# Kernel optimization log

Hardware: AMD Instinct MI355X
Metric: run time of the kernel (lower is better)

Reference implementation:

```python
import jax, jax.numpy as jnp
import numpy as np

THETA = 10000.0
NUM_HEADS = 16


def apply_rope(x, pos, theta):
    # x: [..., s, d_k] with d_k even; pos: [s] (broadcasts over leading dims)
    d_k = x.shape[-1]
    inv_freq = 1.0 / (theta ** (jnp.arange(0, d_k, 2, dtype=x.dtype) / d_k))  # [d_k/2]
    ang = pos.astype(x.dtype)[..., None] * inv_freq  # [s, d_k/2]
    cos, sin = jnp.cos(ang), jnp.sin(ang)
    xr = x.reshape(x.shape[:-1] + (d_k // 2, 2))
    x0, x1 = xr[..., 0], xr[..., 1]
    out0 = x0 * cos - x1 * sin
    out1 = x0 * sin + x1 * cos
    return jnp.stack((out0, out1), axis=-1).reshape(x.shape)


def setup_inputs() -> dict:
    key = jax.random.key(0)
    ks = jax.random.split(key, 5)
    B, S, D = 4, 2048, 1024
    sigma = 2.0 / (D + D) ** 0.5
    return {
        "x": jax.random.normal(ks[0], (B, S, D), dtype=jnp.float32),
        "token_positions": jnp.arange(S, dtype=jnp.int64 if jax.config.jax_enable_x64 else jnp.int32),
        "wq": jax.random.normal(ks[1], (D, D), dtype=jnp.float32) * sigma,
        "wk": jax.random.normal(ks[2], (D, D), dtype=jnp.float32) * sigma,
        "wv": jax.random.normal(ks[3], (D, D), dtype=jnp.float32) * sigma,
        "wo": jax.random.normal(ks[4], (D, D), dtype=jnp.float32) * sigma,
    }


def reference(x, token_positions, wq, wk, wv, wo):
    B, S, D = x.shape
    H = NUM_HEADS
    d_k = D // H

    def proj(w, t):  # weight [out, in], t [..., in]
        return jnp.einsum('oi,bsi->bso', w, t)

    def heads(t):  # [b, s, (h d)] -> [b, h, s, d]
        return t.reshape(B, S, H, d_k).transpose(0, 2, 1, 3)

    Q = heads(proj(wq, x))
    K = heads(proj(wk, x))
    V = heads(proj(wv, x))
    Q = apply_rope(Q, token_positions, THETA)
    K = apply_rope(K, token_positions, THETA)

    scores = jnp.einsum('bhqd,bhkd->bhqk', Q, K) * (d_k ** -0.5)
    causal = jnp.tril(jnp.ones((S, S), dtype=bool))
    scores = jnp.where(causal, scores, -jnp.inf)
    attn = jax.nn.softmax(scores.astype(jnp.float32), axis=-1).astype(scores.dtype)
    out = jnp.einsum('bhqk,bhkd->bhqd', attn, V)
    out = out.transpose(0, 2, 1, 3).reshape(B, S, D)
    return jnp.einsum('oi,bsi->bso', wo, out)
```

## Files before the change

### kernel.cpp

```cpp
#include <hip/hip_runtime.h>
#include <cstdint>
#include <cstddef>

#define Bv 4
#define Sv 2048
#define Hv 16
#define Dv 1024
#define Mv (Bv*Sv)

typedef __attribute__((ext_vector_type(8))) short short8;
typedef __attribute__((ext_vector_type(8))) unsigned short ushort8v;
typedef __attribute__((ext_vector_type(4))) float f32x4;

__device__ inline float bf2f(unsigned short u) {
  union { unsigned int i; float f; } x; x.i = ((unsigned int)u) << 16; return x.f;
}
__device__ inline unsigned short f2bf(float f) {
  union { float f; unsigned int i; } x; x.f = f;
  unsigned int r = x.i + 0x7FFFu + ((x.i >> 16) & 1u);
  return (unsigned short)(r >> 16);
}

typedef __attribute__((address_space(1))) const unsigned short gu16;
typedef __attribute__((address_space(3))) unsigned short lu16;
__device__ inline void gld_lds16(const unsigned short* g, unsigned short* l) {
  __builtin_amdgcn_global_load_lds((gu16*)g, (lu16*)l, 16, 0, 0);
}

__global__ __launch_bounds__(256) void prep_all(
    const float* __restrict__ x, const float* __restrict__ wq,
    const float* __restrict__ wk, const float* __restrict__ wv,
    const float* __restrict__ wo, const int* __restrict__ pos,
    unsigned short* __restrict__ xb, unsigned short* __restrict__ wqkvb,
    unsigned short* __restrict__ wob, float* __restrict__ tab) {
  const int bb = blockIdx.x, tid = threadIdx.x;
  if (bb < 8192) {
    int i = bb * 256 + tid;
    float4 v = reinterpret_cast<const float4*>(x)[i];
    ushort4 o;
    o.x = f2bf(v.x); o.y = f2bf(v.y); o.z = f2bf(v.z); o.w = f2bf(v.w);
    reinterpret_cast<ushort4*>(xb)[i] = o;
  } else if (bb < 11264) {
    int i = (bb - 8192) * 256 + tid;
    int w = i >> 18, off = i & 262143;
    const float* src = (w == 0) ? wq : (w == 1) ? wk : wv;
    float4 v = reinterpret_cast<const float4*>(src)[off];
    ushort4 o;
    o.x = f2bf(v.x); o.y = f2bf(v.y); o.z = f2bf(v.z); o.w = f2bf(v.w);
    reinterpret_cast<ushort4*>(wqkvb)[i] = o;
  } else if (bb < 12288) {
    int i = (bb - 11264) * 256 + tid;
    float4 v = reinterpret_cast<const float4*>(wo)[i];
    ushort4 o;
    o.x = f2bf(v.x); o.y = f2bf(v.y); o.z = f2bf(v.z); o.w = f2bf(v.w);
    reinterpret_cast<ushort4*>(wob)[i] = o;
  } else {
    int idx = (bb - 12288) * 256 + tid;
    int s = idx >> 5, i = idx & 31;
    float p = (float)pos[s];
    float a = p * __builtin_exp2f(-0.41524101186092027f * (float)i);
    tab[(s << 6) + i]      = __builtin_cosf(a);
    tab[(s << 6) + 32 + i] = __builtin_sinf(a);
  }
}

__device__ __forceinline__ void xcd_swizzle(int& bm, int& bn) {
  const int nx = gridDim.x;
  const int nwg = nx * gridDim.y;
  int flat = blockIdx.y * nx + blockIdx.x;
  if ((nwg & 7) == 0) {
    int q = nwg >> 3;
    flat = (flat & 7) * q + (flat >> 3);
  }
  bm = (flat / nx) * 128;
  bn = (flat % nx) * 128;
}

__device__ inline void storeC(float* p, float v) { *p = v; }
__device__ inline void storeC(unsigned short* p, float v) { *p = f2bf(v); }

template <typename CT>
__global__ __launch_bounds__(256) void gemm_bt_128(
    const unsigned short* __restrict__ A,
    const unsigned short* __restrict__ B,
    CT* __restrict__ C,
    int M, int N, int K) {
  __shared__ unsigned short As[128 * 64];
  __shared__ unsigned short Bs[128 * 64];
  const int tid = threadIdx.x;
  const int wave = tid >> 6, lane = tid & 63;
  int bm, bn;
  xcd_swizzle(bm, bn);
  const int wr = (wave >> 1) * 64, wc = (wave & 1) * 64;

  f32x4 acc[4][4] = {};

  int srow[4], scol[4];
#pragma unroll
  for (int i = 0; i < 4; ++i) {
    int c = i * 4 + wave;
    srow[i] = c * 8 + (lane >> 3);
    scol[i] = ((lane & 7) ^ ((lane >> 3) & 7)) * 8;
  }

  const int fr = lane & 15;
  const int g_ = lane >> 4;
  int offA[2][4], offB[2][4];
#pragma unroll
  for (int kh = 0; kh < 2; ++kh)
#pragma unroll
    for (int m = 0; m < 4; ++m) {
      offA[kh][m] = (wr + m * 16 + fr) * 64 + ((((kh << 2) + g_) ^ (fr & 7)) * 8);
      offB[kh][m] = (wc + m * 16 + fr) * 64 + ((((kh << 2) + g_) ^ (fr & 7)) * 8);
    }

  for (int k0 = 0; k0 < K; k0 += 64) {
#pragma unroll
    for (int i = 0; i < 4; ++i) {
      gld_lds16(A + (size_t)(bm + srow[i]) * K + k0 + scol[i], &As[(i * 4 + wave) * 512]);
      gld_lds16(B + (size_t)(bn + srow[i]) * K + k0 + scol[i], &Bs[(i * 4 + wave) * 512]);
    }
    __syncthreads();
#pragma unroll
    for (int kh = 0; kh < 2; ++kh) {
      short8 af[4], bfr[4];
#pragma unroll
      for (int m = 0; m < 4; m++)
        af[m] = *reinterpret_cast<const short8*>(&As[offA[kh][m]]);
#pragma unroll
      for (int n = 0; n < 4; n++)
        bfr[n] = *reinterpret_cast<const short8*>(&Bs[offB[kh][n]]);
#pragma unroll
      for (int m = 0; m < 4; m++)
#pragma unroll
        for (int n = 0; n < 4; n++)
          acc[m][n] = __builtin_amdgcn_mfma_f32_16x16x32_bf16(af[m], bfr[n], acc[m][n], 0, 0, 0);
    }
    __syncthreads();
  }

  const int er = (lane >> 4) * 4, ec = lane & 15;
#pragma unroll
  for (int m = 0; m < 4; m++)
#pragma unroll
    for (int n = 0; n < 4; n++)
#pragma unroll
      for (int r = 0; r < 4; r++) {
        int row = bm + wr + m * 16 + er + r;
        int col = bn + wc + n * 16 + ec;
        storeC(&C[(size_t)row * N + col], acc[m][n][r]);
      }
}

__global__ __launch_bounds__(256) void gemm_qkv(
    const unsigned short* __restrict__ A,
    const unsigned short* __restrict__ B,
    unsigned short* __restrict__ Qp,
    unsigned short* __restrict__ Kp,
    unsigned short* __restrict__ Vt,
    const float* __restrict__ tab) {
  const int K = Dv;
  __shared__ unsigned short As[128 * 64];
  __shared__ unsigned short Bs[128 * 64];
  const int tid = threadIdx.x;
  const int wave = tid >> 6, lane = tid & 63;
  int bm, bn;
  xcd_swizzle(bm, bn);
  const int wr = (wave >> 1) * 64, wc = (wave & 1) * 64;

  f32x4 acc[4][4] = {};

  int srow[4], scol[4];
#pragma unroll
  for (int i = 0; i < 4; ++i) {
    int c = i * 4 + wave;
    srow[i] = c * 8 + (lane >> 3);
    scol[i] = ((lane & 7) ^ ((lane >> 3) & 7)) * 8;
  }

  const int fr = lane & 15;
  const int g_ = lane >> 4;
  int offA[2][4], offB[2][4];
#pragma unroll
  for (int kh = 0; kh < 2; ++kh)
#pragma unroll
    for (int m = 0; m < 4; ++m) {
      offA[kh][m] = (wr + m * 16 + fr) * 64 + ((((kh << 2) + g_) ^ (fr & 7)) * 8);
      offB[kh][m] = (wc + m * 16 + fr) * 64 + ((((kh << 2) + g_) ^ (fr & 7)) * 8);
    }

  for (int k0 = 0; k0 < K; k0 += 64) {
#pragma unroll
    for (int i = 0; i < 4; ++i) {
      gld_lds16(A + (size_t)(bm + srow[i]) * K + k0 + scol[i], &As[(i * 4 + wave) * 512]);
      gld_lds16(B + (size_t)(bn + srow[i]) * K + k0 + scol[i], &Bs[(i * 4 + wave) * 512]);
    }
    __syncthreads();
#pragma unroll
    for (int kh = 0; kh < 2; ++kh) {
      short8 af[4], bfr[4];
#pragma unroll
      for (int m = 0; m < 4; m++)
        af[m] = *reinterpret_cast<const short8*>(&As[offA[kh][m]]);
#pragma unroll
      for (int n = 0; n < 4; n++)
        bfr[n] = *reinterpret_cast<const short8*>(&Bs[offB[kh][n]]);
#pragma unroll
      for (int m = 0; m < 4; m++)
#pragma unroll
        for (int n = 0; n < 4; n++)
          acc[m][n] = __builtin_amdgcn_mfma_f32_16x16x32_bf16(af[m], bfr[n], acc[m][n], 0, 0, 0);
    }
    __syncthreads();
  }

  const int er = (lane >> 4) * 4, ec = lane & 15;
  const int region = bn >> 10;
  if (region < 2) {
    unsigned short* T = (region == 0) ? Qp : Kp;
#pragma unroll
    for (int m = 0; m < 4; m++)
#pragma unroll
      for (int n = 0; n < 4; n++) {
        const int col = bn + wc + n * 16 + ec;
        const int ccol = col & (Dv - 1);
        const int ii = (ccol & 63) >> 1;
        const bool odd = col & 1;
#pragma unroll
        for (int r = 0; r < 4; r++) {
          int row = bm + wr + m * 16 + er + r;
          int s = row & (Sv - 1);
          float v = acc[m][n][r];
          float pv = __shfl_xor(v, 1);
          float cc = tab[(s << 6) + ii];
          float sn = tab[(s << 6) + 32 + ii];
          float o = odd ? __builtin_fmaf(pv, sn, v * cc)
                        : __builtin_fmaf(v, cc, -(pv * sn));
          T[(size_t)row * Dv + ccol] = f2bf(o);
        }
      }
  } else {
#pragma unroll
    for (int m = 0; m < 4; m++)
#pragma unroll
      for (int n = 0; n < 4; n++) {
        const int dfull = (bn - 2048) + wc + n * 16 + ec;
        const int row0 = bm + wr + m * 16 + er;
        const int bb = row0 >> 11, s = row0 & (Sv - 1);
        const size_t vtrow = ((size_t)bb * 16 + (dfull >> 6)) * 64 + (dfull & 63);
        ushort4 ov;
        ov.x = f2bf(acc[m][n][0]);
        ov.y = f2bf(acc[m][n][1]);
        ov.z = f2bf(acc[m][n][2]);
        ov.w = f2bf(acc[m][n][3]);
        *reinterpret_cast<ushort4*>(Vt + vtrow * Sv + s) = ov;
      }
  }
}

template <bool MASKED>
__device__ __forceinline__ void softmax_strip(
    f32x4 (&sacc)[2][4], const int qrel0,
    float (&mrun2)[2], float (&lrun)[2], f32x4 (&oacc)[2][4],
    unsigned int (&pk)[2][4][2]) {
  const float c1 = 0.18033688011112042f;
#pragma unroll
  for (int qf = 0; qf < 2; ++qf) {
    const int qrel = qrel0 + qf * 16;
    float pv[4][4];
    float mx = -INFINITY;
#pragma unroll
    for (int kf = 0; kf < 4; ++kf)
#pragma unroll
      for (int r = 0; r < 4; ++r) {
        float s = sacc[qf][kf][r];
        if (MASKED) s = (kf * 16 + r > qrel) ? -INFINITY : s;
        pv[kf][r] = s;
        mx = fmaxf(mx, s);
      }
    mx = fmaxf(mx, __shfl_xor(mx, 16));
    mx = fmaxf(mx, __shfl_xor(mx, 32));
    float pm = mx * c1;
    if (__any(pm > mrun2[qf] + 8.0f)) {
      float m2 = fmaxf(mrun2[qf], pm);
      float sfq = __builtin_exp2f(mrun2[qf] - m2);
      lrun[qf] *= sfq;
#pragma unroll
      for (int dc = 0; dc < 4; ++dc)
#pragma unroll
        for (int r = 0; r < 4; ++r) oacc[qf][dc][r] *= sfq;
      mrun2[qf] = m2;
    }
    const float nm = -mrun2[qf];
    float ps = 0.f;
#pragma unroll
    for (int kf = 0; kf < 4; ++kf)
#pragma unroll
      for (int r = 0; r < 4; ++r) {
        float p = __builtin_exp2f(__builtin_fmaf(pv[kf][r], c1, nm));
        ps += p;
        pv[kf][r] = p;
      }
    ps += __shfl_xor(ps, 16);
    ps += __shfl_xor(ps, 32);
    lrun[qf] += ps;
#pragma unroll
    for (int kf = 0; kf < 4; ++kf)
#pragma unroll
      for (int hh = 0; hh < 2; ++hh) {
        unsigned int rr;
        asm("v_cvt_pk_bf16_f32 %0, %1, %2"
            : "=v"(rr) : "v"(pv[kf][2 * hh]), "v"(pv[kf][2 * hh + 1]));
        pk[qf][kf][hh] = rr;
      }
  }
}

__device__ __forceinline__ void pv_strip(
    const short8 (&vfr)[2][4], const unsigned int (&pk)[2][4][2],
    f32x4 (&oacc)[2][4], const int idx0, const int idx1, const bool hi) {
#pragma unroll
  for (int ks = 0; ks < 2; ++ks)
#pragma unroll
    for (int qf = 0; qf < 2; ++qf) {
      int ra = __builtin_amdgcn_ds_bpermute(idx0, (int)pk[qf][2 * ks][0]);
      int rb = __builtin_amdgcn_ds_bpermute(idx0, (int)pk[qf][2 * ks + 1][0]);
      int rc = __builtin_amdgcn_ds_bpermute(idx0, (int)pk[qf][2 * ks][1]);
      int rd = __builtin_amdgcn_ds_bpermute(idx0, (int)pk[qf][2 * ks + 1][1]);
      int re = __builtin_amdgcn_ds_bpermute(idx1, (int)pk[qf][2 * ks][0]);
      int rf = __builtin_amdgcn_ds_bpermute(idx1, (int)pk[qf][2 * ks + 1][0]);
      int rg = __builtin_amdgcn_ds_bpermute(idx1, (int)pk[qf][2 * ks][1]);
      int rh = __builtin_amdgcn_ds_bpermute(idx1, (int)pk[qf][2 * ks + 1][1]);
      union { unsigned int u[4]; short8 v; } pw;
      pw.u[0] = hi ? (unsigned)rb : (unsigned)ra;
      pw.u[1] = hi ? (unsigned)rd : (unsigned)rc;
      pw.u[2] = hi ? (unsigned)rf : (unsigned)re;
      pw.u[3] = hi ? (unsigned)rh : (unsigned)rg;
      __builtin_amdgcn_s_setprio(1);
#pragma unroll
      for (int dc = 0; dc < 4; ++dc)
        oacc[qf][dc] = __builtin_amdgcn_mfma_f32_16x16x32_bf16(vfr[ks][dc], pw.v, oacc[qf][dc], 0, 0, 0);
      __builtin_amdgcn_s_setprio(0);
    }
}

__global__ __launch_bounds__(256, 2) void attn_mfma(
    const unsigned short* __restrict__ Q,
    const unsigned short* __restrict__ K,
    const unsigned short* __restrict__ Vt,
    unsigned short* __restrict__ O) {
  __shared__ __align__(16) unsigned short ldsK[3][4096];
  __shared__ __align__(16) unsigned short ldsV[3][4096];
  const int tid = threadIdx.x;
  const int wave = tid >> 6, lane = tid & 63;
  const int g = lane >> 4, m = lane & 15;
  const int F = blockIdx.x;
  const int q7 = F >> 3;
  const int bh = ((F & 7) << 3) | (q7 & 7);
  const int bi = q7 >> 3;
  const int b = bh >> 4, h = bh & 15;
  const int j = bi * 4 + wave;
  const int sA = j, sB = 63 - j;
  const int qA0 = sA * 32, qB0 = sB * 32;
  const int ntA = (sA >> 1) + 1, ntB = (sB >> 1) + 1;
  const int ntBmax = ((63 - bi * 4) >> 1) + 1;
  const size_t qkbase = ((size_t)b * Sv) * Dv + (size_t)h * 64;
  const size_t vtbase = (size_t)bh * 64 * Sv;
  const f32x4 zf = {0.f, 0.f, 0.f, 0.f};

  int srowS[2], scolS[2];
#pragma unroll
  for (int i = 0; i < 2; ++i) {
    int s = ((i * 4 + wave) << 6) + lane;
    int s2 = s ^ ((s >> 3) & 7);
    srowS[i] = s2 >> 3;
    scolS[i] = (s2 & 7) * 8;
  }

  short8 qA[2][2], qB[2][2];
#pragma unroll
  for (int qf = 0; qf < 2; ++qf)
#pragma unroll
    for (int ks = 0; ks < 2; ++ks) {
      qA[qf][ks] = *reinterpret_cast<const short8*>(
          Q + qkbase + (size_t)(qA0 + qf * 16 + m) * Dv + ks * 32 + g * 8);
      qB[qf][ks] = *reinterpret_cast<const short8*>(
          Q + qkbase + (size_t)(qB0 + qf * 16 + m) * Dv + ks * 32 + g * 8);
    }

  int offL[2][4];
#pragma unroll
  for (int ks = 0; ks < 2; ++ks)
#pragma unroll
    for (int f = 0; f < 4; ++f)
      offL[ks][f] = (f * 16 + m) * 64 + ((((ks << 2) + g) ^ (m & 7)) * 8);

  f32x4 oA[2][4] = {}, oB[2][4] = {};
  float mA[2] = {-INFINITY, -INFINITY}, mB[2] = {-INFINITY, -INFINITY};
  float lA[2] = {0.f, 0.f}, lB[2] = {0.f, 0.f};

  const int idx0 = (((g & 1) << 5) + m) << 2;
  const int idx1 = idx0 + 64;
  const bool hi = (g >= 2);
  int qrelA = qA0 + m - 4 * g;
  int qrelB = qB0 + m - 4 * g;

  auto STAGE = [&](int c, int t) {
    const int kb = t << 6;
#pragma unroll
    for (int i = 0; i < 2; ++i) {
      gld_lds16(K + qkbase + (size_t)(kb + srowS[i]) * Dv + scolS[i],
                &ldsK[c][(i * 4 + wave) * 512]);
      gld_lds16(Vt + vtbase + (size_t)srowS[i] * Sv + kb + scolS[i],
                &ldsV[c][(i * 4 + wave) * 512]);
    }
  };

  STAGE(0, 0);
  STAGE(1, 1);
  int cur = 0, bs = 2;

  for (int t = 0; t < ntBmax; ++t) {
    if (t + 1 < ntBmax) {
      asm volatile("s_waitcnt vmcnt(4)" ::: "memory");
    } else {
      asm volatile("s_waitcnt vmcnt(0)" ::: "memory");
    }
    __builtin_amdgcn_sched_barrier(0);
    __builtin_amdgcn_s_barrier();
    if (t + 2 < ntBmax) STAGE(bs, t + 2);

    if (t < ntB) {
      const bool actA = (t < ntA);
      f32x4 sAacc[2][4], sBacc[2][4];
      short8 kfr[4];
#pragma unroll
      for (int kf = 0; kf < 4; ++kf)
        kfr[kf] = *reinterpret_cast<const short8*>(&ldsK[cur][offL[0][kf]]);
      __builtin_amdgcn_s_setprio(1);
#pragma unroll
      for (int qf = 0; qf < 2; ++qf)
#pragma unroll
        for (int kf = 0; kf < 4; ++kf)
          sBacc[qf][kf] = __builtin_amdgcn_mfma_f32_16x16x32_bf16(kfr[kf], qB[qf][0], zf, 0, 0, 0);
      if (actA)
#pragma unroll
        for (int qf = 0; qf < 2; ++qf)
#pragma unroll
          for (int kf = 0; kf < 4; ++kf)
            sAacc[qf][kf] = __builtin_amdgcn_mfma_f32_16x16x32_bf16(kfr[kf], qA[qf][0], zf, 0, 0, 0);
      __builtin_amdgcn_s_setprio(0);
#pragma unroll
      for (int kf = 0; kf < 4; ++kf)
        kfr[kf] = *reinterpret_cast<const short8*>(&ldsK[cur][offL[1][kf]]);
      __builtin_amdgcn_s_setprio(1);
#pragma unroll
      for (int qf = 0; qf < 2; ++qf)
#pragma unroll
        for (int kf = 0; kf < 4; ++kf)
          sBacc[qf][kf] = __builtin_amdgcn_mfma_f32_16x16x32_bf16(kfr[kf], qB[qf][1], sBacc[qf][kf], 0, 0, 0);
      if (actA)
#pragma unroll
        for (int qf = 0; qf < 2; ++qf)
#pragma unroll
          for (int kf = 0; kf < 4; ++kf)
            sAacc[qf][kf] = __builtin_amdgcn_mfma_f32_16x16x32_bf16(kfr[kf], qA[qf][1], sAacc[qf][kf], 0, 0, 0);
      __builtin_amdgcn_s_setprio(0);

      short8 vfr[2][4];
#pragma unroll
      for (int ks = 0; ks < 2; ++ks)
#pragma unroll
        for (int dc = 0; dc < 4; ++dc)
          vfr[ks][dc] = *reinterpret_cast<const short8*>(&ldsV[cur][offL[ks][dc]]);

      unsigned int pkB[2][4][2], pkA[2][4][2];
      if (t == ntB - 1) softmax_strip<true >(sBacc, qrelB, mB, lB, oB, pkB);
      else              softmax_strip<false>(sBacc, qrelB, mB, lB, oB, pkB);
      if (actA) {
        if (t == ntA - 1) softmax_strip<true >(sAacc, qrelA, mA, lA, oA, pkA);
        else              softmax_strip<false>(sAacc, qrelA, mA, lA, oA, pkA);
      }
      pv_strip(vfr, pkB, oB, idx0, idx1, hi);
      if (actA) pv_strip(vfr, pkA, oA, idx0, idx1, hi);

      qrelA -= 64; qrelB -= 64;
    }

    cur = (cur == 2) ? 0 : cur + 1;
    bs = (bs == 2) ? 0 : bs + 1;
  }

#pragma unroll
  for (int qf = 0; qf < 2; ++qf) {
    float rnA = 1.0f / lA[qf];
    float rnB = 1.0f / lB[qf];
    size_t rowA = (size_t)(qA0 + qf * 16 + m);
    size_t rowB = (size_t)(qB0 + qf * 16 + m);
#pragma unroll
    for (int dc = 0; dc < 4; ++dc) {
      ushort4 ov;
      ov.x = f2bf(oA[qf][dc][0] * rnA);
      ov.y = f2bf(oA[qf][dc][1] * rnA);
      ov.z = f2bf(oA[qf][dc][2] * rnA);
      ov.w = f2bf(oA[qf][dc][3] * rnA);
      *reinterpret_cast<ushort4*>(O + qkbase + rowA * Dv + dc * 16 + 4 * g) = ov;
      ov.x = f2bf(oB[qf][dc][0] * rnB);
      ov.y = f2bf(oB[qf][dc][1] * rnB);
      ov.z = f2bf(oB[qf][dc][2] * rnB);
      ov.w = f2bf(oB[qf][dc][3] * rnB);
      *reinterpret_cast<ushort4*>(O + qkbase + rowB * Dv + dc * 16 + 4 * g) = ov;
    }
  }
}

extern "C" void kernel_launch(void* const* d_in, const int* in_sizes, int n_in,
                              void* d_out, int out_size, void* d_ws, size_t ws_size,
                              hipStream_t stream) {
  const float* x   = (const float*)d_in[0];
  const int*   pos = (const int*)d_in[1];
  const float* wq  = (const float*)d_in[2];
  const float* wk  = (const float*)d_in[3];
  const float* wv  = (const float*)d_in[4];
  const float* wo  = (const float*)d_in[5];
  float* out = (float*)d_out;

  char* w = (char*)d_ws;
  unsigned short* xb    = (unsigned short*)(w);
  unsigned short* wqkvb = (unsigned short*)(w + (16u << 20));
  unsigned short* wob   = (unsigned short*)(w + (22u << 20));
  unsigned short* Qp    = (unsigned short*)(w + (24u << 20));
  unsigned short* Kp    = (unsigned short*)(w + (40u << 20));
  unsigned short* Vt    = (unsigned short*)(w + (56u << 20));
  float*          tab   = (float*)(w + (72u << 20));

  prep_all<<<12544, 256, 0, stream>>>(x, wq, wk, wv, wo, pos, xb, wqkvb, wob, tab);

  gemm_qkv<<<dim3(3 * Dv / 128, Mv / 128), 256, 0, stream>>>(xb, wqkvb, Qp, Kp, Vt, tab);

  attn_mfma<<<512, 256, 0, stream>>>(Qp, Kp, Vt, xb);

  gemm_bt_128<float><<<dim3(Dv / 128, Mv / 128), 256, 0, stream>>>(xb, wob, out, Mv, Dv, Dv);
}
```

Before: 201.7 us.

## Split paired causal strips across separate waves with 512-thread attention blocks

The attention block grows from 4 to 8 waves. Each wave now handles a single 32-row query strip, where before one wave handled both a short and a long strip. Waves 0-3 take the front strips and waves 4-7 take the mirrored back strips, and each wave stages one K/V chunk per tile, so the vmcnt wait is adjusted to match. The goal is to halve per-wave register pressure and raise the number of resident waves, giving more latency hiding. The cost is that the short-strip waves sit idle at the barriers while the long-strip waves finish, which makes load imbalance inside a block worse.

```diff
diff --git a/kernel.cpp b/kernel.cpp
--- a/kernel.cpp
+++ b/kernel.cpp
@@ -344,7 +344,7 @@
     }
 }
 
-__global__ __launch_bounds__(256, 2) void attn_mfma(
+__global__ __launch_bounds__(512, 4) void attn_mfma(
     const unsigned short* __restrict__ Q,
     const unsigned short* __restrict__ K,
     const unsigned short* __restrict__ Vt,
@@ -359,34 +359,31 @@
   const int bh = ((F & 7) << 3) | (q7 & 7);
   const int bi = q7 >> 3;
   const int b = bh >> 4, h = bh & 15;
-  const int j = bi * 4 + wave;
-  const int sA = j, sB = 63 - j;
-  const int qA0 = sA * 32, qB0 = sB * 32;
-  const int ntA = (sA >> 1) + 1, ntB = (sB >> 1) + 1;
+  const int w4 = wave & 3;
+  const bool isB = wave >= 4;
+  const int strip = isB ? (63 - (bi * 4 + w4)) : (bi * 4 + w4);
+  const int q0 = strip * 32;
+  const int nt = (strip >> 1) + 1;
   const int ntBmax = ((63 - bi * 4) >> 1) + 1;
   const size_t qkbase = ((size_t)b * Sv) * Dv + (size_t)h * 64;
   const size_t vtbase = (size_t)bh * 64 * Sv;
   const f32x4 zf = {0.f, 0.f, 0.f, 0.f};
 
-  int srowS[2], scolS[2];
-#pragma unroll
-  for (int i = 0; i < 2; ++i) {
-    int s = ((i * 4 + wave) << 6) + lane;
+  int srowS, scolS;
+  {
+    int s = (wave << 6) + lane;
     int s2 = s ^ ((s >> 3) & 7);
-    srowS[i] = s2 >> 3;
-    scolS[i] = (s2 & 7) * 8;
-  }
-
-  short8 qA[2][2], qB[2][2];
+    srowS = s2 >> 3;
+    scolS = (s2 & 7) * 8;
+  }
+
+  short8 q[2][2];
 #pragma unroll
   for (int qf = 0; qf < 2; ++qf)
 #pragma unroll
-    for (int ks = 0; ks < 2; ++ks) {
-      qA[qf][ks] = *reinterpret_cast<const short8*>(
-          Q + qkbase + (size_t)(qA0 + qf * 16 + m) * Dv + ks * 32 + g * 8);
-      qB[qf][ks] = *reinterpret_cast<const short8*>(
-          Q + qkbase + (size_t)(qB0 + qf * 16 + m) * Dv + ks * 32 + g * 8);
-    }
+    for (int ks = 0; ks < 2; ++ks)
+      q[qf][ks] = *reinterpret_cast<const short8*>(
+          Q + qkbase + (size_t)(q0 + qf * 16 + m) * Dv + ks * 32 + g * 8);
 
   int offL[2][4];
 #pragma unroll
@@ -395,25 +392,21 @@
     for (int f = 0; f < 4; ++f)
       offL[ks][f] = (f * 16 + m) * 64 + ((((ks << 2) + g) ^ (m & 7)) * 8);
 
-  f32x4 oA[2][4] = {}, oB[2][4] = {};
-  float mA[2] = {-INFINITY, -INFINITY}, mB[2] = {-INFINITY, -INFINITY};
-  float lA[2] = {0.f, 0.f}, lB[2] = {0.f, 0.f};
+  f32x4 oacc[2][4] = {};
+  float mrun[2] = {-INFINITY, -INFINITY};
+  float lrun[2] = {0.f, 0.f};
 
   const int idx0 = (((g & 1) << 5) + m) << 2;
   const int idx1 = idx0 + 64;
   const bool hi = (g >= 2);
-  int qrelA = qA0 + m - 4 * g;
-  int qrelB = qB0 + m - 4 * g;
+  int qrel = q0 + m - 4 * g;
 
   auto STAGE = [&](int c, int t) {
     const int kb = t << 6;
-#pragma unroll
-    for (int i = 0; i < 2; ++i) {
-      gld_lds16(K + qkbase + (size_t)(kb + srowS[i]) * Dv + scolS[i],
-                &ldsK[c][(i * 4 + wave) * 512]);
-      gld_lds16(Vt + vtbase + (size_t)srowS[i] * Sv + kb + scolS[i],
-                &ldsV[c][(i * 4 + wave) * 512]);
-    }
+    gld_lds16(K + qkbase + (size_t)(kb + srowS) * Dv + scolS,
+              &ldsK[c][wave * 512]);
+    gld_lds16(Vt + vtbase + (size_t)srowS * Sv + kb + scolS,
+              &ldsV[c][wave * 512]);
   };
 
   STAGE(0, 0);
@@ -422,7 +415,7 @@
 
   for (int t = 0; t < ntBmax; ++t) {
     if (t + 1 < ntBmax) {
-      asm volatile("s_waitcnt vmcnt(4)" ::: "memory");
+      asm volatile("s_waitcnt vmcnt(2)" ::: "memory");
     } else {
       asm volatile("s_waitcnt vmcnt(0)" ::: "memory");
     }
@@ -430,9 +423,8 @@
     __builtin_amdgcn_s_barrier();
     if (t + 2 < ntBmax) STAGE(bs, t + 2);
 
-    if (t < ntB) {
-      const bool actA = (t < ntA);
-      f32x4 sAacc[2][4], sBacc[2][4];
+    if (t < nt) {
+      f32x4 sacc[2][4];
       short8 kfr[4];
 #pragma unroll
       for (int kf = 0; kf < 4; ++kf)
@@ -442,13 +434,7 @@
       for (int qf = 0; qf < 2; ++qf)
 #pragma unroll
         for (int kf = 0; kf < 4; ++kf)
-          sBacc[qf][kf] = __builtin_amdgcn_mfma_f32_16x16x32_bf16(kfr[kf], qB[qf][0], zf, 0, 0, 0);
-      if (actA)
-#pragma unroll
-        for (int qf = 0; qf < 2; ++qf)
-#pragma unroll
-          for (int kf = 0; kf < 4; ++kf)
-            sAacc[qf][kf] = __builtin_amdgcn_mfma_f32_16x16x32_bf16(kfr[kf], qA[qf][0], zf, 0, 0, 0);
+          sacc[qf][kf] = __builtin_amdgcn_mfma_f32_16x16x32_bf16(kfr[kf], q[qf][0], zf, 0, 0, 0);
       __builtin_amdgcn_s_setprio(0);
 #pragma unroll
       for (int kf = 0; kf < 4; ++kf)
@@ -458,13 +444,7 @@
       for (int qf = 0; qf < 2; ++qf)
 #pragma unroll
         for (int kf = 0; kf < 4; ++kf)
-          sBacc[qf][kf] = __builtin_amdgcn_mfma_f32_16x16x32_bf16(kfr[kf], qB[qf][1], sBacc[qf][kf], 0, 0, 0);
-      if (actA)
-#pragma unroll
-        for (int qf = 0; qf < 2; ++qf)
-#pragma unroll
-          for (int kf = 0; kf < 4; ++kf)
-            sAacc[qf][kf] = __builtin_amdgcn_mfma_f32_16x16x32_bf16(kfr[kf], qA[qf][1], sAacc[qf][kf], 0, 0, 0);
+          sacc[qf][kf] = __builtin_amdgcn_mfma_f32_16x16x32_bf16(kfr[kf], q[qf][1], sacc[qf][kf], 0, 0, 0);
       __builtin_amdgcn_s_setprio(0);
 
       short8 vfr[2][4];
@@ -474,17 +454,12 @@
         for (int dc = 0; dc < 4; ++dc)
           vfr[ks][dc] = *reinterpret_cast<const short8*>(&ldsV[cur][offL[ks][dc]]);
 
-      unsigned int pkB[2][4][2], pkA[2][4][2];
-      if (t == ntB - 1) softmax_strip<true >(sBacc, qrelB, mB, lB, oB, pkB);
-      else              softmax_strip<false>(sBacc, qrelB, mB, lB, oB, pkB);
-      if (actA) {
-        if (t == ntA - 1) softmax_strip<true >(sAacc, qrelA, mA, lA, oA, pkA);
-        else              softmax_strip<false>(sAacc, qrelA, mA, lA, oA, pkA);
-      }
-      pv_strip(vfr, pkB, oB, idx0, idx1, hi);
-      if (actA) pv_strip(vfr, pkA, oA, idx0, idx1, hi);
-
-      qrelA -= 64; qrelB -= 64;
+      unsigned int pk[2][4][2];
+      if (t == nt - 1) softmax_strip<true >(sacc, qrel, mrun, lrun, oacc, pk);
+      else             softmax_strip<false>(sacc, qrel, mrun, lrun, oacc, pk);
+      pv_strip(vfr, pk, oacc, idx0, idx1, hi);
+
+      qrel -= 64;
     }
 
     cur = (cur == 2) ? 0 : cur + 1;
@@ -493,23 +468,16 @@
 
 #pragma unroll
   for (int qf = 0; qf < 2; ++qf) {
-    float rnA = 1.0f / lA[qf];
-    float rnB = 1.0f / lB[qf];
-    size_t rowA = (size_t)(qA0 + qf * 16 + m);
-    size_t rowB = (size_t)(qB0 + qf * 16 + m);
+    float rn = 1.0f / lrun[qf];
+    size_t row = (size_t)(q0 + qf * 16 + m);
 #pragma unroll
     for (int dc = 0; dc < 4; ++dc) {
       ushort4 ov;
-      ov.x = f2bf(oA[qf][dc][0] * rnA);
-      ov.y = f2bf(oA[qf][dc][1] * rnA);
-      ov.z = f2bf(oA[qf][dc][2] * rnA);
-      ov.w = f2bf(oA[qf][dc][3] * rnA);
-      *reinterpret_cast<ushort4*>(O + qkbase + rowA * Dv + dc * 16 + 4 * g) = ov;
-      ov.x = f2bf(oB[qf][dc][0] * rnB);
-      ov.y = f2bf(oB[qf][dc][1] * rnB);
-      ov.z = f2bf(oB[qf][dc][2] * rnB);
-      ov.w = f2bf(oB[qf][dc][3] * rnB);
-      *reinterpret_cast<ushort4*>(O + qkbase + rowB * Dv + dc * 16 + 4 * g) = ov;
+      ov.x = f2bf(oacc[qf][dc][0] * rn);
+      ov.y = f2bf(oacc[qf][dc][1] * rn);
+      ov.z = f2bf(oacc[qf][dc][2] * rn);
+      ov.w = f2bf(oacc[qf][dc][3] * rn);
+      *reinterpret_cast<ushort4*>(O + qkbase + row * Dv + dc * 16 + 4 * g) = ov;
     }
   }
 }
@@ -538,7 +506,7 @@
 
   gemm_qkv<<<dim3(3 * Dv / 128, Mv / 128), 256, 0, stream>>>(xb, wqkvb, Qp, Kp, Vt, tab);
 
-  attn_mfma<<<512, 256, 0, stream>>>(Qp, Kp, Vt, xb);
+  attn_mfma<<<512, 512, 0, stream>>>(Qp, Kp, Vt, xb);
 
   gemm_bt_128<float><<<dim3(Dv / 128, Mv / 128), 256, 0, stream>>>(xb, wob, out, Mv, Dv, Dv);
 }
```

After: 276.2 us. +36.9%, slower.

## Overlap next K-tile global-to-LDS load with second-half MFMAs in GEMMs

Applied to the files above, without the earlier changes.

Restructures the K loop of the projection GEMMs so the second half-tile fragments are read into registers before a barrier. The next tile's direct global-to-LDS load is then issued while the last 16 MFMAs run on those registers, instead of loading only after all compute finishes. This hides part of the global load latency behind compute while keeping a single LDS buffer. It costs extra registers for the second fragment set, and the loop still has two barriers per tile.

```diff
diff --git a/kernel.cpp b/kernel.cpp
--- a/kernel.cpp
+++ b/kernel.cpp
@@ -114,28 +114,46 @@
       offB[kh][m] = (wc + m * 16 + fr) * 64 + ((((kh << 2) + g_) ^ (fr & 7)) * 8);
     }
 
-  for (int k0 = 0; k0 < K; k0 += 64) {
+  const int nt = K >> 6;
+  auto STAGE = [&](int t) {
+    const int k0 = t << 6;
 #pragma unroll
     for (int i = 0; i < 4; ++i) {
       gld_lds16(A + (size_t)(bm + srow[i]) * K + k0 + scol[i], &As[(i * 4 + wave) * 512]);
       gld_lds16(B + (size_t)(bn + srow[i]) * K + k0 + scol[i], &Bs[(i * 4 + wave) * 512]);
     }
+  };
+
+  STAGE(0);
+  __syncthreads();
+
+  for (int t = 0; t < nt; ++t) {
+    short8 af[4], bfr[4];
+#pragma unroll
+    for (int m = 0; m < 4; m++)
+      af[m] = *reinterpret_cast<const short8*>(&As[offA[0][m]]);
+#pragma unroll
+    for (int n = 0; n < 4; n++)
+      bfr[n] = *reinterpret_cast<const short8*>(&Bs[offB[0][n]]);
+#pragma unroll
+    for (int m = 0; m < 4; m++)
+#pragma unroll
+      for (int n = 0; n < 4; n++)
+        acc[m][n] = __builtin_amdgcn_mfma_f32_16x16x32_bf16(af[m], bfr[n], acc[m][n], 0, 0, 0);
+    short8 af1[4], bf1[4];
+#pragma unroll
+    for (int m = 0; m < 4; m++)
+      af1[m] = *reinterpret_cast<const short8*>(&As[offA[1][m]]);
+#pragma unroll
+    for (int n = 0; n < 4; n++)
+      bf1[n] = *reinterpret_cast<const short8*>(&Bs[offB[1][n]]);
     __syncthreads();
-#pragma unroll
-    for (int kh = 0; kh < 2; ++kh) {
-      short8 af[4], bfr[4];
-#pragma unroll
-      for (int m = 0; m < 4; m++)
-        af[m] = *reinterpret_cast<const short8*>(&As[offA[kh][m]]);
+    if (t + 1 < nt) STAGE(t + 1);
+#pragma unroll
+    for (int m = 0; m < 4; m++)
 #pragma unroll
       for (int n = 0; n < 4; n++)
-        bfr[n] = *reinterpret_cast<const short8*>(&Bs[offB[kh][n]]);
-#pragma unroll
-      for (int m = 0; m < 4; m++)
-#pragma unroll
-        for (int n = 0; n < 4; n++)
-          acc[m][n] = __builtin_amdgcn_mfma_f32_16x16x32_bf16(af[m], bfr[n], acc[m][n], 0, 0, 0);
-    }
+        acc[m][n] = __builtin_amdgcn_mfma_f32_16x16x32_bf16(af1[m], bf1[n], acc[m][n], 0, 0, 0);
     __syncthreads();
   }
 
@@ -189,28 +207,46 @@
       offB[kh][m] = (wc + m * 16 + fr) * 64 + ((((kh << 2) + g_) ^ (fr & 7)) * 8);
     }
 
-  for (int k0 = 0; k0 < K; k0 += 64) {
+  const int nt = K >> 6;
+  auto STAGE = [&](int t) {
+    const int k0 = t << 6;
 #pragma unroll
     for (int i = 0; i < 4; ++i) {
       gld_lds16(A + (size_t)(bm + srow[i]) * K + k0 + scol[i], &As[(i * 4 + wave) * 512]);
       gld_lds16(B + (size_t)(bn + srow[i]) * K + k0 + scol[i], &Bs[(i * 4 + wave) * 512]);
     }
+  };
+
+  STAGE(0);
+  __syncthreads();
+
+  for (int t = 0; t < nt; ++t) {
+    short8 af[4], bfr[4];
+#pragma unroll
+    for (int m = 0; m < 4; m++)
+      af[m] = *reinterpret_cast<const short8*>(&As[offA[0][m]]);
+#pragma unroll
+    for (int n = 0; n < 4; n++)
+      bfr[n] = *reinterpret_cast<const short8*>(&Bs[offB[0][n]]);
+#pragma unroll
+    for (int m = 0; m < 4; m++)
+#pragma unroll
+      for (int n = 0; n < 4; n++)
+        acc[m][n] = __builtin_amdgcn_mfma_f32_16x16x32_bf16(af[m], bfr[n], acc[m][n], 0, 0, 0);
+    short8 af1[4], bf1[4];
+#pragma unroll
+    for (int m = 0; m < 4; m++)
+      af1[m] = *reinterpret_cast<const short8*>(&As[offA[1][m]]);
+#pragma unroll
+    for (int n = 0; n < 4; n++)
+      bf1[n] = *reinterpret_cast<const short8*>(&Bs[offB[1][n]]);
     __syncthreads();
-#pragma unroll
-    for (int kh = 0; kh < 2; ++kh) {
-      short8 af[4], bfr[4];
-#pragma unroll
-      for (int m = 0; m < 4; m++)
-        af[m] = *reinterpret_cast<const short8*>(&As[offA[kh][m]]);
+    if (t + 1 < nt) STAGE(t + 1);
+#pragma unroll
+    for (int m = 0; m < 4; m++)
 #pragma unroll
       for (int n = 0; n < 4; n++)
-        bfr[n] = *reinterpret_cast<const short8*>(&Bs[offB[kh][n]]);
-#pragma unroll
-      for (int m = 0; m < 4; m++)
-#pragma unroll
-        for (int n = 0; n < 4; n++)
-          acc[m][n] = __builtin_amdgcn_mfma_f32_16x16x32_bf16(af[m], bfr[n], acc[m][n], 0, 0, 0);
-    }
+        acc[m][n] = __builtin_amdgcn_mfma_f32_16x16x32_bf16(af1[m], bf1[n], acc[m][n], 0, 0, 0);
     __syncthreads();
   }
 
```

After: 200.6 us, median of 2. No clear change (-0.6%).
